# Optimization experiments

Measured on AMD Instinct MI355X. Metric: run time of the kernel, lower is better.

The kernel has to match this reference:

```python
import jax, jax.numpy as jnp
import numpy as np

N_ENT, N_REL, B, D = 100000, 500, 16, 128
P_NORM = 1
EPS = 1e-12


def _l2_normalize(x):
    # mirrors torch.nn.functional.normalize(x, 2, -1)
    n = jnp.sqrt(jnp.sum(x * x, axis=-1, keepdims=True))
    return x / jnp.maximum(n, EPS)


def setup_inputs() -> dict:
    key = jax.random.key(0)
    k0, k1, k2, k3 = jax.random.split(key, 4)
    # xavier_normal_ init: std = sqrt(2 / (fan_in + fan_out))
    ent_emb = jax.random.normal(k0, (N_ENT, D), dtype=jnp.float32) * np.sqrt(2.0 / (N_ENT + D))
    rel_emb = jax.random.normal(k1, (N_REL, D), dtype=jnp.float32) * np.sqrt(2.0 / (N_REL + D))
    e1 = jax.random.randint(k2, (B,), 0, N_ENT, dtype=jnp.int64)
    rel = jax.random.randint(k3, (B,), 0, N_REL, dtype=jnp.int64)
    X = jnp.zeros((B, D), dtype=jnp.float32)   # unused by forward (as in source)
    A = jnp.zeros((B, B), dtype=jnp.float32)   # unused by forward (as in source)
    return {"e1": e1, "rel": rel, "X": X, "A": A, "ent_emb": ent_emb, "rel_emb": rel_emb}


def reference(e1, rel, X, A, ent_emb, rel_emb) -> jnp.ndarray:
    # e1_embedded = normalize(ent_emb[e1]); rel_embedded = normalize(rel_emb[rel])
    e1_e = _l2_normalize(ent_emb[e1])          # [B, D]
    rel_e = _l2_normalize(rel_emb[rel])        # [B, D]
    node = _l2_normalize(ent_emb)              # [N, D]
    head_add_rel = e1_e + rel_e                # [B, D]
    # broadcast pairwise difference: [B, N, D]
    diff = head_add_rel[:, None, :] - node[None, :, :]
    if P_NORM == 1:
        dist = jnp.sum(jnp.abs(diff), axis=2)              # [B, N]
    else:
        dist = jnp.sum(jnp.abs(diff) ** P_NORM, axis=2) ** (1.0 / P_NORM)
    # loss_name == 'BCELoss' -> softmax over entities
    pred = jax.nn.softmax(dist, axis=-1)       # [B, N]
    return pred
```

## Files before the change

kernel.cpp:

```cpp
#include <hip/hip_runtime.h>
#include <hip/hip_bf16.h>

#define N_ENT 100000
#define NB 16
#define DIM 128
#define TILE 64
#define RSTRIDE 132
#define NBLK 768
#define N_TILES ((N_ENT + TILE - 1) / TILE)

__global__ __launch_bounds__(128) void head_kernel(
    const int* __restrict__ e1, const int* __restrict__ rel,
    const float* __restrict__ ent, const float* __restrict__ relemb,
    float* __restrict__ head)
{
    int b = blockIdx.x, d = threadIdx.x;
    float ev = ent[e1[b] * DIM + d];
    float rv = relemb[rel[b] * DIM + d];
    __shared__ float s1[DIM], s2[DIM];
    s1[d] = ev * ev;
    s2[d] = rv * rv;
    __syncthreads();
    for (int s = 64; s > 0; s >>= 1) {
        if (d < s) { s1[d] += s1[d + s]; s2[d] += s2[d + s]; }
        __syncthreads();
    }
    float ne = fmaxf(sqrtf(s1[0]), 1e-12f);
    float nr = fmaxf(sqrtf(s2[0]), 1e-12f);
    head[b * DIM + d] = ev / ne + rv / nr;
}

__global__ __launch_bounds__(256) void dist_kernel(
    const float* __restrict__ ent, const float* __restrict__ head,
    float* __restrict__ partials, float* __restrict__ out)
{
    __shared__ float ldsRow[TILE * RSTRIDE];
    __shared__ float ldsHead[NB * DIM];
    __shared__ float ldsInv[TILE];

    const int tid  = threadIdx.x;
    const int lane = tid & 63;
    const int wv   = tid >> 6;
    const int bbase = wv * 4;

    {
        const float4* hg = (const float4*)head;
        float4* hl = (float4*)ldsHead;
        hl[tid]       = hg[tid];
        hl[tid + 256] = hg[tid + 256];
    }

    float es0 = 0.f, es1 = 0.f, es2 = 0.f, es3 = 0.f;

    for (int tile = blockIdx.x; tile < N_TILES; tile += NBLK) {
        const int n0 = tile * TILE;
        __syncthreads();

        {
            const float4* eg = (const float4*)ent;
            #pragma unroll
            for (int i = 0; i < 8; i++) {
                int g = tid + i * 256;
                int r = g >> 5, c = g & 31;
                int gr = n0 + r;
                if (gr >= N_ENT) gr = N_ENT - 1;
                float4 v = eg[gr * (DIM / 4) + c];
                *(float4*)&ldsRow[r * RSTRIDE + c * 4] = v;
            }
        }
        __syncthreads();

        {
            int r = tid >> 2, q = tid & 3;
            const float* p = &ldsRow[r * RSTRIDE + q * 32];
            float s = 0.f;
            #pragma unroll
            for (int k = 0; k < 8; k++) {
                float4 v = *(const float4*)&p[k * 4];
                s = fmaf(v.x, v.x, s); s = fmaf(v.y, v.y, s);
                s = fmaf(v.z, v.z, s); s = fmaf(v.w, v.w, s);
            }
            s += __shfl_down(s, 2);
            s += __shfl_down(s, 1);
            if (q == 0) ldsInv[r] = 1.0f / fmaxf(sqrtf(s), 1e-12f);
        }
        __syncthreads();

        const float inv = ldsInv[lane];
        const float* rp = &ldsRow[lane * RSTRIDE];
        const float4* h0 = (const float4*)&ldsHead[(bbase + 0) * DIM];
        const float4* h1 = (const float4*)&ldsHead[(bbase + 1) * DIM];
        const float4* h2 = (const float4*)&ldsHead[(bbase + 2) * DIM];
        const float4* h3 = (const float4*)&ldsHead[(bbase + 3) * DIM];

        float a0 = 0.f, a1 = 0.f, a2 = 0.f, a3 = 0.f;
        #pragma unroll 4
        for (int j = 0; j < DIM / 4; j++) {
            float4 v  = *(const float4*)&rp[j * 4];
            float4 q0 = h0[j], q1 = h1[j], q2 = h2[j], q3 = h3[j];
            a0 += fabsf(fmaf(-v.x, inv, q0.x)) + fabsf(fmaf(-v.y, inv, q0.y))
                + fabsf(fmaf(-v.z, inv, q0.z)) + fabsf(fmaf(-v.w, inv, q0.w));
            a1 += fabsf(fmaf(-v.x, inv, q1.x)) + fabsf(fmaf(-v.y, inv, q1.y))
                + fabsf(fmaf(-v.z, inv, q1.z)) + fabsf(fmaf(-v.w, inv, q1.w));
            a2 += fabsf(fmaf(-v.x, inv, q2.x)) + fabsf(fmaf(-v.y, inv, q2.y))
                + fabsf(fmaf(-v.z, inv, q2.z)) + fabsf(fmaf(-v.w, inv, q2.w));
            a3 += fabsf(fmaf(-v.x, inv, q3.x)) + fabsf(fmaf(-v.y, inv, q3.y))
                + fabsf(fmaf(-v.z, inv, q3.z)) + fabsf(fmaf(-v.w, inv, q3.w));
        }

        const int n = n0 + lane;
        const bool valid = (n < N_ENT);
        float e0 = valid ? __expf(a0) : 0.f;
        float e1 = valid ? __expf(a1) : 0.f;
        float e2 = valid ? __expf(a2) : 0.f;
        float e3 = valid ? __expf(a3) : 0.f;
        if (valid) {
            out[(bbase + 0) * N_ENT + n] = e0;
            out[(bbase + 1) * N_ENT + n] = e1;
            out[(bbase + 2) * N_ENT + n] = e2;
            out[(bbase + 3) * N_ENT + n] = e3;
        }
        es0 += e0; es1 += e1; es2 += e2; es3 += e3;
    }

#define WRED(x) { x += __shfl_down(x, 32); x += __shfl_down(x, 16); \
                  x += __shfl_down(x, 8);  x += __shfl_down(x, 4);  \
                  x += __shfl_down(x, 2);  x += __shfl_down(x, 1); }
    WRED(es0) WRED(es1) WRED(es2) WRED(es3)
#undef WRED
    if (lane == 0) {
        partials[(bbase + 0) * NBLK + blockIdx.x] = es0;
        partials[(bbase + 1) * NBLK + blockIdx.x] = es1;
        partials[(bbase + 2) * NBLK + blockIdx.x] = es2;
        partials[(bbase + 3) * NBLK + blockIdx.x] = es3;
    }
}

__global__ __launch_bounds__(64) void reduce_kernel(
    const float* __restrict__ partials, float* __restrict__ rowsum)
{
    const int b = blockIdx.x;
    const int lane = threadIdx.x;
    float s = 0.f;
    for (int k = lane; k < NBLK; k += 64) s += partials[b * NBLK + k];
    s += __shfl_down(s, 32); s += __shfl_down(s, 16);
    s += __shfl_down(s, 8);  s += __shfl_down(s, 4);
    s += __shfl_down(s, 2);  s += __shfl_down(s, 1);
    if (lane == 0) rowsum[b] = s;
}

__global__ __launch_bounds__(256) void scale_kernel(
    float* __restrict__ out, const float* __restrict__ rowsum)
{
    const int b = blockIdx.y;
    const float invS = 1.0f / rowsum[b];
    const int i = blockIdx.x * 256 + threadIdx.x;
    if (i < N_ENT / 4) {
        float4* row = (float4*)&out[b * N_ENT];
        float4 v = row[i];
        v.x *= invS; v.y *= invS; v.z *= invS; v.w *= invS;
        row[i] = v;
    }
}

extern "C" void kernel_launch(void* const* d_in, const int* in_sizes, int n_in,
                              void* d_out, int out_size, void* d_ws, size_t ws_size,
                              hipStream_t stream) {
    const int*   e1     = (const int*)d_in[0];
    const int*   rel    = (const int*)d_in[1];
    const float* ent    = (const float*)d_in[4];
    const float* relemb = (const float*)d_in[5];
    float* out = (float*)d_out;

    float* head     = (float*)d_ws;
    float* partials = (float*)((char*)d_ws + 8192);
    float* rowsum   = (float*)((char*)d_ws + 8192 + 49152);

    head_kernel<<<16, 128, 0, stream>>>(e1, rel, ent, relemb, head);
    dist_kernel<<<NBLK, 256, 0, stream>>>(ent, head, partials, out);
    reduce_kernel<<<NB, 64, 0, stream>>>(partials, rowsum);
    scale_kernel<<<dim3((N_ENT / 4 + 255) / 256, NB), 256, 0, stream>>>(out, rowsum);
}
```

Baseline: 121.7 us.

## Fuse partial-sum reduction into scale kernel and read head via scalar loads

```diff
diff --git a/kernel.cpp b/kernel.cpp
--- a/kernel.cpp
+++ b/kernel.cpp
@@ -6,7 +6,7 @@
 #define DIM 128
 #define TILE 64
 #define RSTRIDE 132
-#define NBLK 768
+#define NBLK 1024
 #define N_TILES ((N_ENT + TILE - 1) / TILE)
 
 __global__ __launch_bounds__(128) void head_kernel(
@@ -35,20 +35,13 @@
     float* __restrict__ partials, float* __restrict__ out)
 {
     __shared__ float ldsRow[TILE * RSTRIDE];
-    __shared__ float ldsHead[NB * DIM];
     __shared__ float ldsInv[TILE];
 
     const int tid  = threadIdx.x;
     const int lane = tid & 63;
-    const int wv   = tid >> 6;
+    const int wv   = __builtin_amdgcn_readfirstlane(tid >> 6);
     const int bbase = wv * 4;
-
-    {
-        const float4* hg = (const float4*)head;
-        float4* hl = (float4*)ldsHead;
-        hl[tid]       = hg[tid];
-        hl[tid + 256] = hg[tid + 256];
-    }
+    const float4* __restrict__ hg = (const float4*)head;
 
     float es0 = 0.f, es1 = 0.f, es2 = 0.f, es3 = 0.f;
 
@@ -88,16 +81,15 @@
 
         const float inv = ldsInv[lane];
         const float* rp = &ldsRow[lane * RSTRIDE];
-        const float4* h0 = (const float4*)&ldsHead[(bbase + 0) * DIM];
-        const float4* h1 = (const float4*)&ldsHead[(bbase + 1) * DIM];
-        const float4* h2 = (const float4*)&ldsHead[(bbase + 2) * DIM];
-        const float4* h3 = (const float4*)&ldsHead[(bbase + 3) * DIM];
 
         float a0 = 0.f, a1 = 0.f, a2 = 0.f, a3 = 0.f;
-        #pragma unroll 4
+        #pragma unroll 8
         for (int j = 0; j < DIM / 4; j++) {
             float4 v  = *(const float4*)&rp[j * 4];
-            float4 q0 = h0[j], q1 = h1[j], q2 = h2[j], q3 = h3[j];
+            float4 q0 = hg[(bbase + 0) * (DIM / 4) + j];
+            float4 q1 = hg[(bbase + 1) * (DIM / 4) + j];
+            float4 q2 = hg[(bbase + 2) * (DIM / 4) + j];
+            float4 q3 = hg[(bbase + 3) * (DIM / 4) + j];
             a0 += fabsf(fmaf(-v.x, inv, q0.x)) + fabsf(fmaf(-v.y, inv, q0.y))
                 + fabsf(fmaf(-v.z, inv, q0.z)) + fabsf(fmaf(-v.w, inv, q0.w));
             a1 += fabsf(fmaf(-v.x, inv, q1.x)) + fabsf(fmaf(-v.y, inv, q1.y))
@@ -136,28 +128,30 @@
     }
 }
 
-__global__ __launch_bounds__(64) void reduce_kernel(
-    const float* __restrict__ partials, float* __restrict__ rowsum)
+__global__ __launch_bounds__(256) void scale_kernel(
+    float* __restrict__ out, const float* __restrict__ partials)
 {
-    const int b = blockIdx.x;
-    const int lane = threadIdx.x;
+    const int b = blockIdx.y;
+    const int tid = threadIdx.x;
+
+    const int i = blockIdx.x * 256 + tid;
+    float4 v = make_float4(0.f, 0.f, 0.f, 0.f);
+    float4* row = (float4*)&out[b * N_ENT];
+    const bool valid = (i < N_ENT / 4);
+    if (valid) v = row[i];
+
     float s = 0.f;
-    for (int k = lane; k < NBLK; k += 64) s += partials[b * NBLK + k];
+    #pragma unroll
+    for (int k = 0; k < NBLK / 256; k++) s += partials[b * NBLK + k * 256 + tid];
     s += __shfl_down(s, 32); s += __shfl_down(s, 16);
     s += __shfl_down(s, 8);  s += __shfl_down(s, 4);
     s += __shfl_down(s, 2);  s += __shfl_down(s, 1);
-    if (lane == 0) rowsum[b] = s;
-}
+    __shared__ float red[4];
+    if ((tid & 63) == 0) red[tid >> 6] = s;
+    __syncthreads();
+    const float invS = 1.0f / (red[0] + red[1] + red[2] + red[3]);
 
-__global__ __launch_bounds__(256) void scale_kernel(
-    float* __restrict__ out, const float* __restrict__ rowsum)
-{
-    const int b = blockIdx.y;
-    const float invS = 1.0f / rowsum[b];
-    const int i = blockIdx.x * 256 + threadIdx.x;
-    if (i < N_ENT / 4) {
-        float4* row = (float4*)&out[b * N_ENT];
-        float4 v = row[i];
+    if (valid) {
         v.x *= invS; v.y *= invS; v.z *= invS; v.w *= invS;
         row[i] = v;
     }
@@ -174,10 +168,8 @@
 
     float* head     = (float*)d_ws;
     float* partials = (float*)((char*)d_ws + 8192);
-    float* rowsum   = (float*)((char*)d_ws + 8192 + 49152);
 
     head_kernel<<<16, 128, 0, stream>>>(e1, rel, ent, relemb, head);
     dist_kernel<<<NBLK, 256, 0, stream>>>(ent, head, partials, out);
-    reduce_kernel<<<NB, 64, 0, stream>>>(partials, rowsum);
-    scale_kernel<<<dim3((N_ENT / 4 + 255) / 256, NB), 256, 0, stream>>>(out, rowsum);
+    scale_kernel<<<dim3((N_ENT / 4 + 255) / 256, NB), 256, 0, stream>>>(out, partials);
 }
```

After: 113.3 us. 6.8% less time.
